# Kernel optimization log

Hardware: AMD Instinct MI355X
Metric: run time of the kernel (lower is better)

Reference implementation:

```python
import jax, jax.numpy as jnp
import numpy as np

N_NODES = 50000
N_EDGES = 640000
D_IN = 128
D_HID = 128
D_OUT = 128
N_GRAPHS = 64


def gcn_conv(x, edge_index, W, b, n_nodes):
    """PyG GCNConv: D^{-1/2} (A + I) D^{-1/2} X W + b (unit edge weights)."""
    src, dst = edge_index[0], edge_index[1]
    h = x @ W  # [N, d_out]
    # degree counts target-side edges plus the self loop
    deg = jax.ops.segment_sum(jnp.ones_like(dst, dtype=h.dtype), dst,
                              num_segments=n_nodes) + 1.0
    dinv = jax.lax.rsqrt(deg)  # deg >= 1 so always finite
    norm = dinv[src] * dinv[dst]  # [E]
    msg = h[src] * norm[:, None]  # gather + scale  [E, d_out]
    agg = jax.ops.segment_sum(msg, dst, num_segments=n_nodes)
    # self-loop contribution: norm_ii = dinv_i^2
    agg = agg + h * (dinv * dinv)[:, None]
    return agg + b


def global_mean_pool(x, batch, n_graphs):
    sums = jax.ops.segment_sum(x, batch, num_segments=n_graphs)
    cnt = jax.ops.segment_sum(jnp.ones((x.shape[0],), dtype=x.dtype), batch,
                              num_segments=n_graphs)
    return sums / jnp.maximum(cnt, 1.0)[:, None]


def setup_inputs() -> dict:
    key = jax.random.key(0)
    k = jax.random.split(key, 8)
    x = jax.random.normal(k[0], (N_NODES, D_IN), dtype=jnp.float32)
    edge_index = jax.random.randint(k[1], (2, N_EDGES), 0, N_NODES, dtype=jnp.int64)
    batch = jnp.sort(jax.random.randint(k[2], (N_NODES,), 0, N_GRAPHS, dtype=jnp.int64))
    s1 = 1.0 / np.sqrt(D_IN)
    s2 = 1.0 / np.sqrt(D_HID)
    W1 = jax.random.uniform(k[3], (D_IN, D_HID), jnp.float32, -s1, s1)
    b1 = jnp.zeros((D_HID,), jnp.float32)
    W2 = jax.random.uniform(k[4], (D_HID, D_OUT), jnp.float32, -s2, s2)
    b2 = jnp.zeros((D_OUT,), jnp.float32)
    return {"x": x, "edge_index": edge_index, "batch": batch,
            "W1": W1, "b1": b1, "W2": W2, "b2": b2}


def reference(x, edge_index, batch, W1, b1, W2, b2):
    n = x.shape[0]
    h = jax.nn.relu(gcn_conv(x, edge_index, W1, b1, n))
    h = gcn_conv(h, edge_index, W2, b2, n)
    return global_mean_pool(h, batch, N_GRAPHS)
```

## Files before the change

### kernel.cpp

```cpp
#include <hip/hip_runtime.h>


#define D 128
#define NGRAPH 64
#define AGG_BLOCKS 2048
#define BUCK_SH 9
#define BUCK_W  512
#define MAXBUCK 128

typedef _Float16 h16x2 __attribute__((ext_vector_type(2)));
typedef _Float16 f16x8 __attribute__((ext_vector_type(8)));
typedef float    f32x4 __attribute__((ext_vector_type(4)));
typedef unsigned short u16x8 __attribute__((ext_vector_type(8)));

__device__ __forceinline__ float2 h2f(unsigned u) {
    h16x2 h = __builtin_bit_cast(h16x2, u);
    return make_float2((float)h.x, (float)h.y);
}
__device__ __forceinline__ unsigned f2h(float x, float y) {
    h16x2 h;
    h.x = (_Float16)x;
    h.y = (_Float16)y;
    return __builtin_bit_cast(unsigned, h);
}

__global__ void zero_out_kernel(float* __restrict__ out, int n) {
    int i = blockIdx.x * blockDim.x + threadIdx.x;
    if (i < n) out[i] = 0.f;
}

__global__ __launch_bounds__(256) void pack_scatter_kernel(const float* __restrict__ W1,
                                                           _Float16* __restrict__ WB,
                                                           const int* __restrict__ ei,
                                                           int* __restrict__ bcnt,
                                                           unsigned* __restrict__ buck,
                                                           unsigned* __restrict__ Gz,
                                                           unsigned* __restrict__ Hz,
                                                           int N, int E, int CAP) {
    int b = (int)blockIdx.x;
    int t = (int)threadIdx.x;
    if (b < 8) {
        int idx = b * 256 + t;
        int lane = idx & 63;
        int nt   = (idx >> 6) & 7;
        int kt   = idx >> 9;
        int col  = nt * 16 + (lane & 15);
        int krow = kt * 32 + (lane >> 4) * 8;
#pragma unroll
        for (int j = 0; j < 8; ++j)
            WB[idx * 8 + j] = (_Float16)W1[(krow + j) * D + col];
        return;
    }
    if (b == 8) {
        if (t < 64)       Gz[(size_t)N * 64 + t] = 0u;
        else if (t < 128) Hz[(size_t)N * 64 + (t - 64)] = 0u;
        return;
    }
    __shared__ unsigned histL[MAXBUCK];
    __shared__ int      baseL[MAXBUCK];
    if (t < MAXBUCK) histL[t] = 0u;
    __syncthreads();

    int e0 = (b - 9) * 1024;
    int bid[4];
    unsigned lidx[4], pk[4];
#pragma unroll
    for (int j = 0; j < 4; ++j) {
        int e = e0 + t + j * 256;
        bid[j] = -1;
        if (e < E) {
            int s = ei[e];
            int d = ei[E + e];
            if (d >= 0 && d < N) {
                s = min(max(s, 0), N - 1);
                bid[j] = d >> BUCK_SH;
                pk[j]  = ((unsigned)d << 16) | (unsigned)s;
            }
        }
    }
#pragma unroll
    for (int j = 0; j < 4; ++j)
        if (bid[j] >= 0) lidx[j] = atomicAdd(&histL[bid[j]], 1u);
    __syncthreads();
    if (t < MAXBUCK && histL[t] > 0u)
        baseL[t] = atomicAdd(&bcnt[t], (int)histL[t]);
    __syncthreads();
#pragma unroll
    for (int j = 0; j < 4; ++j)
        if (bid[j] >= 0) {
            int slot = baseL[bid[j]] + (int)lidx[j];
            if (slot < CAP) buck[(size_t)bid[j] * CAP + slot] = pk[j];
        }
}

__global__ __launch_bounds__(256) void bucket_deg_kernel(const unsigned* __restrict__ buck,
                                                         const int* __restrict__ bcnt,
                                                         int* __restrict__ deg,
                                                         float* __restrict__ dinv,
                                                         int* __restrict__ padsum,
                                                         int N, int CAP) {
    __shared__ int degL[BUCK_W];
    __shared__ int red[256];
    int b = (int)blockIdx.x;
    int t = (int)threadIdx.x;
    for (int k = t; k < BUCK_W; k += 256) degL[k] = 0;
    __syncthreads();
    int cnt = min(bcnt[b], CAP);
    const unsigned* bp = buck + (size_t)b * CAP;
    for (int i = t; i < cnt; i += 256)
        atomicAdd(&degL[(bp[i] >> 16) & (BUCK_W - 1)], 1);
    __syncthreads();
    int base = b << BUCK_SH;
    int local = 0;
    for (int k = t; k < BUCK_W; k += 256) {
        int d = base + k;
        if (d < N) {
            int dg = degL[k];
            deg[d]  = dg;
            dinv[d] = rsqrtf((float)dg + 1.0f);
            local  += (dg + 7) & ~7;
        }
    }
    red[t] = local;
    __syncthreads();
    for (int off = 128; off > 0; off >>= 1) {
        if (t < off) red[t] += red[t + off];
        __syncthreads();
    }
    if (t == 0) padsum[b] = red[0];
}

__global__ __launch_bounds__(128) void bucket_scan_kernel(const int* __restrict__ padsum,
                                                          int* __restrict__ bbase,
                                                          int* __restrict__ rowstart,
                                                          int N, int nbuck) {
    __shared__ int s[128];
    int t = (int)threadIdx.x;
    int own = (t < nbuck) ? padsum[t] : 0;
    s[t] = own;
    __syncthreads();
    for (int off = 1; off < 128; off <<= 1) {
        int v = (t >= off) ? s[t - off] : 0;
        __syncthreads();
        s[t] += v;
        __syncthreads();
    }
    if (t < nbuck) bbase[t] = s[t] - own;
    if (t == 127) rowstart[N] = s[127];
}

__global__ __launch_bounds__(256) void gemm_fill_kernel(const float* __restrict__ X,
                                                        const _Float16* __restrict__ WB,
                                                        const float* __restrict__ dinv,
                                                        _Float16* __restrict__ Gh,
                                                        const unsigned* __restrict__ buck,
                                                        const int* __restrict__ bcnt,
                                                        const int* __restrict__ deg,
                                                        const int* __restrict__ bbase,
                                                        int* __restrict__ rowstart,
                                                        unsigned short* __restrict__ colidx,
                                                        int N, int CAP, int gb) {
    if ((int)blockIdx.x >= gb) {
        __shared__ int degS[BUCK_W];
        __shared__ int loff[BUCK_W];
        __shared__ int sc[256];
        int b = (int)blockIdx.x - gb;
        int t = (int)threadIdx.x;
        int base_d = b << BUCK_SH;
        for (int k = t; k < BUCK_W; k += 256) {
            int d = base_d + k;
            degS[k] = (d < N) ? deg[d] : 0;
        }
        __syncthreads();
        int p0 = (degS[2 * t] + 7) & ~7;
        int p1 = (degS[2 * t + 1] + 7) & ~7;
        int own = p0 + p1;
        sc[t] = own;
        __syncthreads();
        for (int off = 1; off < 256; off <<= 1) {
            int v = (t >= off) ? sc[t - off] : 0;
            __syncthreads();
            sc[t] += v;
            __syncthreads();
        }
        int excl = sc[t] - own;
        loff[2 * t]     = excl;
        loff[2 * t + 1] = excl + p0;
        __syncthreads();
        int bb = bbase[b];
        for (int k = t; k < BUCK_W; k += 256) {
            int d = base_d + k;
            if (d < N) {
                int rs = bb + loff[k];
                rowstart[d] = rs;
                int dg = degS[k];
                int p8 = (dg + 7) & ~7;
                for (int j = dg; j < p8; ++j)
                    colidx[rs + j] = (unsigned short)N;
            }
        }
        __syncthreads();
        for (int k = t; k < BUCK_W; k += 256) degS[k] = bb + loff[k];
        __syncthreads();
        int cnt = min(bcnt[b], CAP);
        const unsigned* bp = buck + (size_t)b * CAP;
        for (int i = t; i < cnt; i += 256) {
            unsigned u = bp[i];
            int ld = (int)((u >> 16) & (BUCK_W - 1));
            int slot = atomicAdd(&degS[ld], 1);
            colidx[slot] = (unsigned short)(u & 0xffffu);
        }
        return;
    }

    int t = (int)threadIdx.x;
    int wave = t >> 6, lane = t & 63;
    int mbase = blockIdx.x * 64 + wave * 16;
    int arow  = mbase + (lane & 15);
    if (arow >= N) arow = N - 1;
    int kgrp  = lane >> 4;

    f16x8 afrag[4];
#pragma unroll
    for (int kt = 0; kt < 4; ++kt) {
        const float* xp = X + (size_t)arow * D + kt * 32 + kgrp * 8;
        float4 a0 = *(const float4*)xp;
        float4 a1 = *(const float4*)(xp + 4);
        f16x8 af;
        af[0] = (_Float16)a0.x; af[1] = (_Float16)a0.y;
        af[2] = (_Float16)a0.z; af[3] = (_Float16)a0.w;
        af[4] = (_Float16)a1.x; af[5] = (_Float16)a1.y;
        af[6] = (_Float16)a1.z; af[7] = (_Float16)a1.w;
        afrag[kt] = af;
    }
    f32x4 acc[8];
#pragma unroll
    for (int nt = 0; nt < 8; ++nt) acc[nt] = (f32x4){0.f, 0.f, 0.f, 0.f};
#pragma unroll
    for (int kt = 0; kt < 4; ++kt) {
#pragma unroll
        for (int nt = 0; nt < 8; ++nt) {
            uint4 u = *(const uint4*)(WB + (((kt * 8 + nt) * 64 + lane) * 8));
            f16x8 bfrag = __builtin_bit_cast(f16x8, u);
            acc[nt] = __builtin_amdgcn_mfma_f32_16x16x32_f16(afrag[kt], bfrag, acc[nt], 0, 0, 0);
        }
    }
    int r0 = mbase + kgrp * 4;
#pragma unroll
    for (int r = 0; r < 4; ++r) {
        int row = r0 + r;
        if (row < N) {
            float dv = dinv[row];
#pragma unroll
            for (int nt = 0; nt < 8; ++nt)
                Gh[(size_t)row * D + nt * 16 + (lane & 15)] = (_Float16)(dv * acc[nt][r]);
        }
    }
}

__global__ __launch_bounds__(256) void agg1_kernel(const unsigned* __restrict__ Gh,
                                                   const int* __restrict__ rowstart,
                                                   const unsigned short* __restrict__ colidx,
                                                   const float* __restrict__ dinv,
                                                   const float* __restrict__ b1,
                                                   unsigned* __restrict__ Hh,
                                                   int N, int chunk) {
    int gid  = blockIdx.x * 4 + (threadIdx.x >> 6);
    int lane = threadIdx.x & 63;
    int i0 = gid * chunk, i1 = min(i0 + chunk, N);
    float bx = b1[2 * lane], by = b1[2 * lane + 1];
    for (int i = i0; i < i1; ++i) {
        float di = dinv[i];
        float2 acc = h2f(Gh[(size_t)i * 64 + lane]);
        int e0 = rowstart[i], e1 = rowstart[i + 1];
        for (int e = e0; e < e1; e += 8) {
            u16x8 cc = *(const u16x8*)(colidx + e);
            unsigned u[8];
#pragma unroll
            for (int j = 0; j < 8; ++j)
                u[j] = Gh[(size_t)cc[j] * 64 + lane];
#pragma unroll
            for (int j = 0; j < 8; ++j) {
                float2 v = h2f(u[j]);
                acc.x += v.x;
                acc.y += v.y;
            }
        }
        float hx = fmaxf(fmaf(di, acc.x, bx), 0.f) * di;
        float hy = fmaxf(fmaf(di, acc.y, by), 0.f) * di;
        Hh[(size_t)i * 64 + lane] = f2h(hx, hy);
    }
}

__global__ __launch_bounds__(256) void agg2_pool_kernel(const unsigned* __restrict__ Hh,
                                                        const int* __restrict__ rowstart,
                                                        const unsigned short* __restrict__ colidx,
                                                        const float* __restrict__ dinv,
                                                        const int* __restrict__ batch,
                                                        float* __restrict__ pool,
                                                        int N, int chunk) {
    int gid  = blockIdx.x * 4 + (threadIdx.x >> 6);
    int lane = threadIdx.x & 63;
    int i0 = gid * chunk, i1 = min(i0 + chunk, N);
    if (i0 >= N) return;

    float2 pa = make_float2(0.f, 0.f);
    int cur = min(max(batch[i0], 0), NGRAPH - 1);
    for (int i = i0; i < i1; ++i) {
        float di = dinv[i];
        float2 a = h2f(Hh[(size_t)i * 64 + lane]);
        int e0 = rowstart[i], e1 = rowstart[i + 1];
        for (int e = e0; e < e1; e += 8) {
            u16x8 cc = *(const u16x8*)(colidx + e);
            unsigned u[8];
#pragma unroll
            for (int j = 0; j < 8; ++j)
                u[j] = Hh[(size_t)cc[j] * 64 + lane];
#pragma unroll
            for (int j = 0; j < 8; ++j) {
                float2 v = h2f(u[j]);
                a.x += v.x;
                a.y += v.y;
            }
        }
        int b = min(max(batch[i], 0), NGRAPH - 1);
        if (b != cur) {
            atomicAdd(&pool[(size_t)cur * D + 2 * lane], pa.x);
            atomicAdd(&pool[(size_t)cur * D + 2 * lane + 1], pa.y);
            pa = make_float2(0.f, 0.f);
            cur = b;
        }
        pa.x = fmaf(di, a.x, pa.x);
        pa.y = fmaf(di, a.y, pa.y);
    }
    atomicAdd(&pool[(size_t)cur * D + 2 * lane], pa.x);
    atomicAdd(&pool[(size_t)cur * D + 2 * lane + 1], pa.y);
}

__device__ __forceinline__ int lbound(const int* __restrict__ a, int n, int v) {
    int lo = 0, hi = n;
    while (lo < hi) {
        int m = (lo + hi) >> 1;
        if (a[m] < v) lo = m + 1; else hi = m;
    }
    return lo;
}

__global__ void final_gemm_kernel(const float* __restrict__ pool,
                                  const int* __restrict__ batch,
                                  const float* __restrict__ W2,
                                  const float* __restrict__ b2,
                                  float* __restrict__ out, int N) {
    int g = blockIdx.x, o = threadIdx.x;
    int s = lbound(batch, N, g);
    int e = lbound(batch, N, g + 1);
    float inv_cnt = 1.0f / fmaxf((float)(e - s), 1.0f);
    float acc = 0.f;
#pragma unroll 4
    for (int k = 0; k < D; ++k)
        acc = fmaf(pool[g * D + k], W2[k * D + o], acc);
    out[g * D + o] = acc * inv_cnt + b2[o];
}


extern "C" void kernel_launch(void* const* d_in, const int* in_sizes, int n_in,
                              void* d_out, int out_size, void* d_ws, size_t ws_size,
                              hipStream_t stream) {
    const float* x     = (const float*)d_in[0];
    const int*   ei    = (const int*)  d_in[1];
    const int*   batch = (const int*)  d_in[2];
    const float* W1    = (const float*)d_in[3];
    const float* b1    = (const float*)d_in[4];
    const float* W2    = (const float*)d_in[5];
    const float* b2    = (const float*)d_in[6];
    float* out = (float*)d_out;

    const int N = in_sizes[0] / D;
    const int E = in_sizes[1] / 2;
    const int nbuck = (N + BUCK_W - 1) >> BUCK_SH;
    const int CAP   = (E / (nbuck > 0 ? nbuck : 1)) * 2 + 1024;

    char* ws = (char*)d_ws;
    size_t off = 0;
    auto carve = [&](size_t bytes) {
        size_t o = off;
        off = (off + bytes + 255) & ~(size_t)255;
        return o;
    };
    size_t o_bcnt     = carve((size_t)MAXBUCK * 4);
    size_t o_pool     = carve((size_t)NGRAPH * D * 4);
    size_t zspan      = off;
    size_t o_rowstart = carve((size_t)(N + 1) * 4);
    size_t o_deg      = carve((size_t)N * 4);
    size_t o_dinv     = carve((size_t)N * 4);
    size_t o_padsum   = carve((size_t)MAXBUCK * 4);
    size_t o_bbase    = carve((size_t)MAXBUCK * 4);
    size_t o_colidx   = carve(((size_t)E + 7 * (size_t)N + 64) * 2);
    size_t o_buck     = carve((size_t)nbuck * CAP * 4);
    size_t o_wb       = carve((size_t)D * D * 2);
    size_t o_gh       = carve((size_t)(N + 1) * D * 2);
    size_t o_hh       = carve((size_t)(N + 1) * D * 2);
    size_t need = off;

    if (ws_size < need) {
        zero_out_kernel<<<(out_size + 255) / 256, 256, 0, stream>>>(out, out_size);
        return;
    }

    int*            bcnt     = (int*)           (ws + o_bcnt);
    float*          pool     = (float*)         (ws + o_pool);
    int*            rowstart = (int*)           (ws + o_rowstart);
    int*            deg      = (int*)           (ws + o_deg);
    float*          dinv     = (float*)         (ws + o_dinv);
    int*            padsum   = (int*)           (ws + o_padsum);
    int*            bbase    = (int*)           (ws + o_bbase);
    unsigned short* colidx   = (unsigned short*)(ws + o_colidx);
    unsigned*       buck     = (unsigned*)      (ws + o_buck);
    _Float16*       WB       = (_Float16*)      (ws + o_wb);
    _Float16*       Gh       = (_Float16*)      (ws + o_gh);
    _Float16*       Hh       = (_Float16*)      (ws + o_hh);

    hipMemsetAsync(ws, 0, zspan, stream);

    int ebs = (E + 1023) / 1024;
    int gb  = (N + 63) / 64;

    pack_scatter_kernel<<<9 + ebs, 256, 0, stream>>>(W1, WB, ei, bcnt, buck,
                                                     (unsigned*)Gh, (unsigned*)Hh,
                                                     N, E, CAP);
    bucket_deg_kernel<<<nbuck, 256, 0, stream>>>(buck, bcnt, deg, dinv, padsum, N, CAP);
    bucket_scan_kernel<<<1, 128, 0, stream>>>(padsum, bbase, rowstart, N, nbuck);
    gemm_fill_kernel<<<gb + nbuck, 256, 0, stream>>>(x, WB, dinv, Gh, buck, bcnt,
                                                     deg, bbase, rowstart, colidx,
                                                     N, CAP, gb);

    int groups = AGG_BLOCKS * 4;
    int chunk  = (N + groups - 1) / groups;
    agg1_kernel<<<AGG_BLOCKS, 256, 0, stream>>>((const unsigned*)Gh, rowstart, colidx,
                                                dinv, b1, (unsigned*)Hh, N, chunk);
    agg2_pool_kernel<<<AGG_BLOCKS, 256, 0, stream>>>((const unsigned*)Hh, rowstart, colidx,
                                                     dinv, batch, pool, N, chunk);
    final_gemm_kernel<<<NGRAPH, D, 0, stream>>>(pool, batch, W2, b2, out, N);
}
```

Before: 196.4 us.

## Split feature matrices into column panels and fuse bucket scan into degree kernel

Stores the fp16 feature matrices G and H as four 32-column panels so each block's gathers touch only a 64-byte slice per neighbor, which is meant to improve cache locality. Within a wavefront, four 16-lane groups each gather a different pair of neighbors and combine their partial sums with shuffles. The separate single-block scan kernel is folded into bucket_deg using a last-block ticket, which removes one launch. Each block now handles one panel over more rows, so the per-node serial loop gets longer, and the edge-index loads are repeated across panels.

Result: slower. 269.6 us (+37.2%).

```diff
diff --git a/kernel.cpp b/kernel.cpp
--- a/kernel.cpp
+++ b/kernel.cpp
@@ -4,6 +4,7 @@
 #define D 128
 #define NGRAPH 64
 #define AGG_BLOCKS 2048
+#define NPAN 4
 #define BUCK_SH 9
 #define BUCK_W  512
 #define MAXBUCK 128
@@ -52,8 +53,14 @@
         return;
     }
     if (b == 8) {
-        if (t < 64)       Gz[(size_t)N * 64 + t] = 0u;
-        else if (t < 128) Hz[(size_t)N * 64 + (t - 64)] = 0u;
+        size_t Nrow = (size_t)N + 1;
+        if (t < 64) {
+            int p = t >> 4, k = t & 15;
+            Gz[((size_t)p * Nrow + N) * 16 + k] = 0u;
+        } else if (t < 128) {
+            int q = t - 64, p = q >> 4, k = q & 15;
+            Hz[((size_t)p * Nrow + N) * 16 + k] = 0u;
+        }
         return;
     }
     __shared__ unsigned histL[MAXBUCK];
@@ -98,9 +105,13 @@
                                                          int* __restrict__ deg,
                                                          float* __restrict__ dinv,
                                                          int* __restrict__ padsum,
-                                                         int N, int CAP) {
+                                                         int* __restrict__ bbase,
+                                                         int* __restrict__ rowstart,
+                                                         int* __restrict__ ticket,
+                                                         int N, int CAP, int nbuck) {
     __shared__ int degL[BUCK_W];
     __shared__ int red[256];
+    __shared__ int lastFlag;
     int b = (int)blockIdx.x;
     int t = (int)threadIdx.x;
     for (int k = t; k < BUCK_W; k += 256) degL[k] = 0;
@@ -128,25 +139,24 @@
         __syncthreads();
     }
     if (t == 0) padsum[b] = red[0];
-}
-
-__global__ __launch_bounds__(128) void bucket_scan_kernel(const int* __restrict__ padsum,
-                                                          int* __restrict__ bbase,
-                                                          int* __restrict__ rowstart,
-                                                          int N, int nbuck) {
-    __shared__ int s[128];
-    int t = (int)threadIdx.x;
-    int own = (t < nbuck) ? padsum[t] : 0;
-    s[t] = own;
-    __syncthreads();
-    for (int off = 1; off < 128; off <<= 1) {
-        int v = (t >= off) ? s[t - off] : 0;
-        __syncthreads();
-        s[t] += v;
-        __syncthreads();
-    }
-    if (t < nbuck) bbase[t] = s[t] - own;
-    if (t == 127) rowstart[N] = s[127];
+    __threadfence();
+    if (t == 0) lastFlag = (atomicAdd(ticket, 1) == nbuck - 1) ? 1 : 0;
+    __syncthreads();
+    if (lastFlag) {
+        __threadfence();
+        __shared__ int s[128];
+        int own = (t < nbuck) ? padsum[t] : 0;
+        if (t < 128) s[t] = own;
+        __syncthreads();
+        for (int off = 1; off < 128; off <<= 1) {
+            int v = (t < 128 && t >= off) ? s[t - off] : 0;
+            __syncthreads();
+            if (t < 128) s[t] += v;
+            __syncthreads();
+        }
+        if (t < nbuck) bbase[t] = s[t] - own;
+        if (t == 127) rowstart[N] = s[127];
+    }
 }
 
 __global__ __launch_bounds__(256) void gemm_fill_kernel(const float* __restrict__ X,
@@ -245,6 +255,7 @@
             acc[nt] = __builtin_amdgcn_mfma_f32_16x16x32_f16(afrag[kt], bfrag, acc[nt], 0, 0, 0);
         }
     }
+    size_t Nrow = (size_t)N + 1;
     int r0 = mbase + kgrp * 4;
 #pragma unroll
     for (int r = 0; r < 4; ++r) {
@@ -252,89 +263,124 @@
         if (row < N) {
             float dv = dinv[row];
 #pragma unroll
-            for (int nt = 0; nt < 8; ++nt)
-                Gh[(size_t)row * D + nt * 16 + (lane & 15)] = (_Float16)(dv * acc[nt][r]);
-        }
-    }
-}
-
-__global__ __launch_bounds__(256) void agg1_kernel(const unsigned* __restrict__ Gh,
+            for (int nt = 0; nt < 8; ++nt) {
+                size_t adr = ((size_t)(nt >> 1) * Nrow + row) * 32 + (nt & 1) * 16 + (lane & 15);
+                Gh[adr] = (_Float16)(dv * acc[nt][r]);
+            }
+        }
+    }
+}
+
+__global__ __launch_bounds__(256) void agg1_kernel(const unsigned* __restrict__ Gp,
                                                    const int* __restrict__ rowstart,
                                                    const unsigned short* __restrict__ colidx,
                                                    const float* __restrict__ dinv,
                                                    const float* __restrict__ b1,
-                                                   unsigned* __restrict__ Hh,
+                                                   unsigned* __restrict__ Hp,
                                                    int N, int chunk) {
-    int gid  = blockIdx.x * 4 + (threadIdx.x >> 6);
-    int lane = threadIdx.x & 63;
+    int bid  = (int)blockIdx.x;
+    int p    = bid & (NPAN - 1);
+    int gid  = (bid >> 2) * 4 + ((int)threadIdx.x >> 6);
+    int lane = (int)threadIdx.x & 63;
+    int eq   = lane >> 4;
+    int cl   = lane & 15;
+    size_t Nrow = (size_t)N + 1;
+    const unsigned* P = Gp + (size_t)p * Nrow * 16;
+    unsigned*       H = Hp + (size_t)p * Nrow * 16;
+    float bx = b1[p * 32 + 2 * cl], by = b1[p * 32 + 2 * cl + 1];
     int i0 = gid * chunk, i1 = min(i0 + chunk, N);
-    float bx = b1[2 * lane], by = b1[2 * lane + 1];
+    if (i0 >= N) return;
+    int e = rowstart[i0];
     for (int i = i0; i < i1; ++i) {
         float di = dinv[i];
-        float2 acc = h2f(Gh[(size_t)i * 64 + lane]);
-        int e0 = rowstart[i], e1 = rowstart[i + 1];
-        for (int e = e0; e < e1; e += 8) {
+        int e1 = rowstart[i + 1];
+        float2 acc = make_float2(0.f, 0.f);
+        if (eq == 0) {
+            float2 v = h2f(P[(size_t)i * 16 + cl]);
+            acc.x = v.x; acc.y = v.y;
+        }
+        for (; e < e1; e += 8) {
             u16x8 cc = *(const u16x8*)(colidx + e);
-            unsigned u[8];
-#pragma unroll
-            for (int j = 0; j < 8; ++j)
-                u[j] = Gh[(size_t)cc[j] * 64 + lane];
-#pragma unroll
-            for (int j = 0; j < 8; ++j) {
-                float2 v = h2f(u[j]);
-                acc.x += v.x;
-                acc.y += v.y;
-            }
-        }
-        float hx = fmaxf(fmaf(di, acc.x, bx), 0.f) * di;
-        float hy = fmaxf(fmaf(di, acc.y, by), 0.f) * di;
-        Hh[(size_t)i * 64 + lane] = f2h(hx, hy);
-    }
-}
-
-__global__ __launch_bounds__(256) void agg2_pool_kernel(const unsigned* __restrict__ Hh,
+            int cA = (int)cc[eq];
+            int cB = (int)cc[eq + 4];
+            unsigned uA = P[(size_t)cA * 16 + cl];
+            unsigned uB = P[(size_t)cB * 16 + cl];
+            float2 vA = h2f(uA), vB = h2f(uB);
+            acc.x += vA.x + vB.x;
+            acc.y += vA.y + vB.y;
+        }
+        acc.x += __shfl_xor(acc.x, 16);
+        acc.x += __shfl_xor(acc.x, 32);
+        acc.y += __shfl_xor(acc.y, 16);
+        acc.y += __shfl_xor(acc.y, 32);
+        if (eq == 0) {
+            float hx = fmaxf(fmaf(di, acc.x, bx), 0.f) * di;
+            float hy = fmaxf(fmaf(di, acc.y, by), 0.f) * di;
+            H[(size_t)i * 16 + cl] = f2h(hx, hy);
+        }
+    }
+}
+
+__global__ __launch_bounds__(256) void agg2_pool_kernel(const unsigned* __restrict__ Hp,
                                                         const int* __restrict__ rowstart,
                                                         const unsigned short* __restrict__ colidx,
                                                         const float* __restrict__ dinv,
                                                         const int* __restrict__ batch,
                                                         float* __restrict__ pool,
                                                         int N, int chunk) {
-    int gid  = blockIdx.x * 4 + (threadIdx.x >> 6);
-    int lane = threadIdx.x & 63;
+    int bid  = (int)blockIdx.x;
+    int p    = bid & (NPAN - 1);
+    int gid  = (bid >> 2) * 4 + ((int)threadIdx.x >> 6);
+    int lane = (int)threadIdx.x & 63;
+    int eq   = lane >> 4;
+    int cl   = lane & 15;
+    size_t Nrow = (size_t)N + 1;
+    const unsigned* P = Hp + (size_t)p * Nrow * 16;
     int i0 = gid * chunk, i1 = min(i0 + chunk, N);
     if (i0 >= N) return;
 
     float2 pa = make_float2(0.f, 0.f);
     int cur = min(max(batch[i0], 0), NGRAPH - 1);
+    int e = rowstart[i0];
     for (int i = i0; i < i1; ++i) {
         float di = dinv[i];
-        float2 a = h2f(Hh[(size_t)i * 64 + lane]);
-        int e0 = rowstart[i], e1 = rowstart[i + 1];
-        for (int e = e0; e < e1; e += 8) {
+        int e1 = rowstart[i + 1];
+        float2 acc = make_float2(0.f, 0.f);
+        if (eq == 0) {
+            float2 v = h2f(P[(size_t)i * 16 + cl]);
+            acc.x = v.x; acc.y = v.y;
+        }
+        for (; e < e1; e += 8) {
             u16x8 cc = *(const u16x8*)(colidx + e);
-            unsigned u[8];
-#pragma unroll
-            for (int j = 0; j < 8; ++j)
-                u[j] = Hh[(size_t)cc[j] * 64 + lane];
-#pragma unroll
-            for (int j = 0; j < 8; ++j) {
-                float2 v = h2f(u[j]);
-                a.x += v.x;
-                a.y += v.y;
-            }
-        }
+            int cA = (int)cc[eq];
+            int cB = (int)cc[eq + 4];
+            unsigned uA = P[(size_t)cA * 16 + cl];
+            unsigned uB = P[(size_t)cB * 16 + cl];
+            float2 vA = h2f(uA), vB = h2f(uB);
+            acc.x += vA.x + vB.x;
+            acc.y += vA.y + vB.y;
+        }
+        acc.x += __shfl_xor(acc.x, 16);
+        acc.x += __shfl_xor(acc.x, 32);
+        acc.y += __shfl_xor(acc.y, 16);
+        acc.y += __shfl_xor(acc.y, 32);
+
         int b = min(max(batch[i], 0), NGRAPH - 1);
         if (b != cur) {
-            atomicAdd(&pool[(size_t)cur * D + 2 * lane], pa.x);
-            atomicAdd(&pool[(size_t)cur * D + 2 * lane + 1], pa.y);
+            if (eq == 0) {
+                atomicAdd(&pool[(size_t)cur * D + p * 32 + 2 * cl],     pa.x);
+                atomicAdd(&pool[(size_t)cur * D + p * 32 + 2 * cl + 1], pa.y);
+            }
             pa = make_float2(0.f, 0.f);
             cur = b;
         }
-        pa.x = fmaf(di, a.x, pa.x);
-        pa.y = fmaf(di, a.y, pa.y);
-    }
-    atomicAdd(&pool[(size_t)cur * D + 2 * lane], pa.x);
-    atomicAdd(&pool[(size_t)cur * D + 2 * lane + 1], pa.y);
+        pa.x = fmaf(di, acc.x, pa.x);
+        pa.y = fmaf(di, acc.y, pa.y);
+    }
+    if (eq == 0) {
+        atomicAdd(&pool[(size_t)cur * D + p * 32 + 2 * cl],     pa.x);
+        atomicAdd(&pool[(size_t)cur * D + p * 32 + 2 * cl + 1], pa.y);
+    }
 }
 
 __device__ __forceinline__ int lbound(const int* __restrict__ a, int n, int v) {
@@ -389,6 +435,7 @@
     };
     size_t o_bcnt     = carve((size_t)MAXBUCK * 4);
     size_t o_pool     = carve((size_t)NGRAPH * D * 4);
+    size_t o_ticket   = carve((size_t)256);
     size_t zspan      = off;
     size_t o_rowstart = carve((size_t)(N + 1) * 4);
     size_t o_deg      = carve((size_t)N * 4);
@@ -409,6 +456,7 @@
 
     int*            bcnt     = (int*)           (ws + o_bcnt);
     float*          pool     = (float*)         (ws + o_pool);
+    int*            ticket   = (int*)           (ws + o_ticket);
     int*            rowstart = (int*)           (ws + o_rowstart);
     int*            deg      = (int*)           (ws + o_deg);
     float*          dinv     = (float*)         (ws + o_dinv);
@@ -428,14 +476,14 @@
     pack_scatter_kernel<<<9 + ebs, 256, 0, stream>>>(W1, WB, ei, bcnt, buck,
                                                      (unsigned*)Gh, (unsigned*)Hh,
                                                      N, E, CAP);
-    bucket_deg_kernel<<<nbuck, 256, 0, stream>>>(buck, bcnt, deg, dinv, padsum, N, CAP);
-    bucket_scan_kernel<<<1, 128, 0, stream>>>(padsum, bbase, rowstart, N, nbuck);
+    bucket_deg_kernel<<<nbuck, 256, 0, stream>>>(buck, bcnt, deg, dinv, padsum,
+                                                 bbase, rowstart, ticket,
+                                                 N, CAP, nbuck);
     gemm_fill_kernel<<<gb + nbuck, 256, 0, stream>>>(x, WB, dinv, Gh, buck, bcnt,
                                                      deg, bbase, rowstart, colidx,
                                                      N, CAP, gb);
 
-    int groups = AGG_BLOCKS * 4;
-    int chunk  = (N + groups - 1) / groups;
+    int chunk = (N + AGG_BLOCKS - 1) / AGG_BLOCKS;
     agg1_kernel<<<AGG_BLOCKS, 256, 0, stream>>>((const unsigned*)Gh, rowstart, colidx,
                                                 dinv, b1, (unsigned*)Hh, N, chunk);
     agg2_pool_kernel<<<AGG_BLOCKS, 256, 0, stream>>>((const unsigned*)Hh, rowstart, colidx,
```

## Fuse bucket scan into degree kernel and unroll aggregation gathers with fdot2

Applied to the files above, without the earlier changes.

Merges the single-block prefix-scan kernel into the bucket degree kernel using a last-block ticket counter, which removes one kernel launch. The aggregation loops in both GCN layers now gather 16 neighbours per iteration instead of 8, use 32-bit unsigned index arithmetic, and accumulate fp16 pairs via the fdot2 builtin instead of separate converts and adds. Together these aim to cut launch overhead, raise memory-level parallelism in the gathers and trim the ALU work per element. The cost is more registers per thread and a threadfence/atomic handshake in the degree kernel.

New measurement: 201.4 us. +2.5%, slower.

```diff
diff --git a/kernel.cpp b/kernel.cpp
--- a/kernel.cpp
+++ b/kernel.cpp
@@ -22,6 +22,18 @@
     h.x = (_Float16)x;
     h.y = (_Float16)y;
     return __builtin_bit_cast(unsigned, h);
+}
+__device__ __forceinline__ void fmix2(float& ax, float& ay, unsigned u) {
+    h16x2 h = __builtin_bit_cast(h16x2, u);
+#if __has_builtin(__builtin_amdgcn_fdot2)
+    const h16x2 onelo = {(_Float16)1.0f, (_Float16)0.0f};
+    const h16x2 onehi = {(_Float16)0.0f, (_Float16)1.0f};
+    ax = __builtin_amdgcn_fdot2(h, onelo, ax, false);
+    ay = __builtin_amdgcn_fdot2(h, onehi, ay, false);
+#else
+    ax += (float)h.x;
+    ay += (float)h.y;
+#endif
 }
 
 __global__ void zero_out_kernel(float* __restrict__ out, int n) {
@@ -98,9 +110,13 @@
                                                          int* __restrict__ deg,
                                                          float* __restrict__ dinv,
                                                          int* __restrict__ padsum,
-                                                         int N, int CAP) {
+                                                         int* __restrict__ bbase,
+                                                         int* __restrict__ rowstart,
+                                                         int* __restrict__ ticket,
+                                                         int N, int CAP, int nbuck) {
     __shared__ int degL[BUCK_W];
     __shared__ int red[256];
+    __shared__ int lastFlag;
     int b = (int)blockIdx.x;
     int t = (int)threadIdx.x;
     for (int k = t; k < BUCK_W; k += 256) degL[k] = 0;
@@ -128,25 +144,24 @@
         __syncthreads();
     }
     if (t == 0) padsum[b] = red[0];
-}
-
-__global__ __launch_bounds__(128) void bucket_scan_kernel(const int* __restrict__ padsum,
-                                                          int* __restrict__ bbase,
-                                                          int* __restrict__ rowstart,
-                                                          int N, int nbuck) {
-    __shared__ int s[128];
-    int t = (int)threadIdx.x;
-    int own = (t < nbuck) ? padsum[t] : 0;
-    s[t] = own;
-    __syncthreads();
-    for (int off = 1; off < 128; off <<= 1) {
-        int v = (t >= off) ? s[t - off] : 0;
-        __syncthreads();
-        s[t] += v;
-        __syncthreads();
-    }
-    if (t < nbuck) bbase[t] = s[t] - own;
-    if (t == 127) rowstart[N] = s[127];
+    __threadfence();
+    if (t == 0) lastFlag = (atomicAdd(ticket, 1) == nbuck - 1) ? 1 : 0;
+    __syncthreads();
+    if (lastFlag) {
+        __threadfence();
+        __shared__ int s[128];
+        int own = (t < nbuck) ? padsum[t] : 0;
+        if (t < 128) s[t] = own;
+        __syncthreads();
+        for (int off = 1; off < 128; off <<= 1) {
+            int v = (t < 128 && t >= off) ? s[t - off] : 0;
+            __syncthreads();
+            if (t < 128) s[t] += v;
+            __syncthreads();
+        }
+        if (t < nbuck) bbase[t] = s[t] - own;
+        if (t == 127) rowstart[N] = s[127];
+    }
 }
 
 __global__ __launch_bounds__(256) void gemm_fill_kernel(const float* __restrict__ X,
@@ -266,29 +281,40 @@
                                                    unsigned* __restrict__ Hh,
                                                    int N, int chunk) {
     int gid  = blockIdx.x * 4 + (threadIdx.x >> 6);
-    int lane = threadIdx.x & 63;
+    unsigned lane = threadIdx.x & 63;
     int i0 = gid * chunk, i1 = min(i0 + chunk, N);
     float bx = b1[2 * lane], by = b1[2 * lane + 1];
     for (int i = i0; i < i1; ++i) {
         float di = dinv[i];
-        float2 acc = h2f(Gh[(size_t)i * 64 + lane]);
+        float ax = 0.f, ay = 0.f;
+        fmix2(ax, ay, Gh[((unsigned)i << 6) + lane]);
         int e0 = rowstart[i], e1 = rowstart[i + 1];
-        for (int e = e0; e < e1; e += 8) {
+        int e = e0;
+        for (; e + 15 < e1; e += 16) {
+            u16x8 c0 = *(const u16x8*)(colidx + e);
+            u16x8 c1 = *(const u16x8*)(colidx + e + 8);
+            unsigned u[16];
+#pragma unroll
+            for (int j = 0; j < 8; ++j)
+                u[j] = Gh[((unsigned)c0[j] << 6) + lane];
+#pragma unroll
+            for (int j = 0; j < 8; ++j)
+                u[8 + j] = Gh[((unsigned)c1[j] << 6) + lane];
+#pragma unroll
+            for (int j = 0; j < 16; ++j) fmix2(ax, ay, u[j]);
+        }
+        for (; e < e1; e += 8) {
             u16x8 cc = *(const u16x8*)(colidx + e);
             unsigned u[8];
 #pragma unroll
             for (int j = 0; j < 8; ++j)
-                u[j] = Gh[(size_t)cc[j] * 64 + lane];
-#pragma unroll
-            for (int j = 0; j < 8; ++j) {
-                float2 v = h2f(u[j]);
-                acc.x += v.x;
-                acc.y += v.y;
-            }
-        }
-        float hx = fmaxf(fmaf(di, acc.x, bx), 0.f) * di;
-        float hy = fmaxf(fmaf(di, acc.y, by), 0.f) * di;
-        Hh[(size_t)i * 64 + lane] = f2h(hx, hy);
+                u[j] = Gh[((unsigned)cc[j] << 6) + lane];
+#pragma unroll
+            for (int j = 0; j < 8; ++j) fmix2(ax, ay, u[j]);
+        }
+        float hx = fmaxf(fmaf(di, ax, bx), 0.f) * di;
+        float hy = fmaxf(fmaf(di, ay, by), 0.f) * di;
+        Hh[((unsigned)i << 6) + lane] = f2h(hx, hy);
     }
 }
 
@@ -300,7 +326,7 @@
                                                         float* __restrict__ pool,
                                                         int N, int chunk) {
     int gid  = blockIdx.x * 4 + (threadIdx.x >> 6);
-    int lane = threadIdx.x & 63;
+    unsigned lane = threadIdx.x & 63;
     int i0 = gid * chunk, i1 = min(i0 + chunk, N);
     if (i0 >= N) return;
 
@@ -308,20 +334,31 @@
     int cur = min(max(batch[i0], 0), NGRAPH - 1);
     for (int i = i0; i < i1; ++i) {
         float di = dinv[i];
-        float2 a = h2f(Hh[(size_t)i * 64 + lane]);
+        float ax = 0.f, ay = 0.f;
+        fmix2(ax, ay, Hh[((unsigned)i << 6) + lane]);
         int e0 = rowstart[i], e1 = rowstart[i + 1];
-        for (int e = e0; e < e1; e += 8) {
+        int e = e0;
+        for (; e + 15 < e1; e += 16) {
+            u16x8 c0 = *(const u16x8*)(colidx + e);
+            u16x8 c1 = *(const u16x8*)(colidx + e + 8);
+            unsigned u[16];
+#pragma unroll
+            for (int j = 0; j < 8; ++j)
+                u[j] = Hh[((unsigned)c0[j] << 6) + lane];
+#pragma unroll
+            for (int j = 0; j < 8; ++j)
+                u[8 + j] = Hh[((unsigned)c1[j] << 6) + lane];
+#pragma unroll
+            for (int j = 0; j < 16; ++j) fmix2(ax, ay, u[j]);
+        }
+        for (; e < e1; e += 8) {
             u16x8 cc = *(const u16x8*)(colidx + e);
             unsigned u[8];
 #pragma unroll
             for (int j = 0; j < 8; ++j)
-                u[j] = Hh[(size_t)cc[j] * 64 + lane];
-#pragma unroll
-            for (int j = 0; j < 8; ++j) {
-                float2 v = h2f(u[j]);
-                a.x += v.x;
-                a.y += v.y;
-            }
+                u[j] = Hh[((unsigned)cc[j] << 6) + lane];
+#pragma unroll
+            for (int j = 0; j < 8; ++j) fmix2(ax, ay, u[j]);
         }
         int b = min(max(batch[i], 0), NGRAPH - 1);
         if (b != cur) {
@@ -330,8 +367,8 @@
             pa = make_float2(0.f, 0.f);
             cur = b;
         }
-        pa.x = fmaf(di, a.x, pa.x);
-        pa.y = fmaf(di, a.y, pa.y);
+        pa.x = fmaf(di, ax, pa.x);
+        pa.y = fmaf(di, ay, pa.y);
     }
     atomicAdd(&pool[(size_t)cur * D + 2 * lane], pa.x);
     atomicAdd(&pool[(size_t)cur * D + 2 * lane + 1], pa.y);
@@ -389,6 +426,7 @@
     };
     size_t o_bcnt     = carve((size_t)MAXBUCK * 4);
     size_t o_pool     = carve((size_t)NGRAPH * D * 4);
+    size_t o_ticket   = carve((size_t)256);
     size_t zspan      = off;
     size_t o_rowstart = carve((size_t)(N + 1) * 4);
     size_t o_deg      = carve((size_t)N * 4);
@@ -409,6 +447,7 @@
 
     int*            bcnt     = (int*)           (ws + o_bcnt);
     float*          pool     = (float*)         (ws + o_pool);
+    int*            ticket   = (int*)           (ws + o_ticket);
     int*            rowstart = (int*)           (ws + o_rowstart);
     int*            deg      = (int*)           (ws + o_deg);
     float*          dinv     = (float*)         (ws + o_dinv);
@@ -428,8 +467,9 @@
     pack_scatter_kernel<<<9 + ebs, 256, 0, stream>>>(W1, WB, ei, bcnt, buck,
                                                      (unsigned*)Gh, (unsigned*)Hh,
                                                      N, E, CAP);
-    bucket_deg_kernel<<<nbuck, 256, 0, stream>>>(buck, bcnt, deg, dinv, padsum, N, CAP);
-    bucket_scan_kernel<<<1, 128, 0, stream>>>(padsum, bbase, rowstart, N, nbuck);
+    bucket_deg_kernel<<<nbuck, 256, 0, stream>>>(buck, bcnt, deg, dinv, padsum,
+                                                 bbase, rowstart, ticket,
+                                                 N, CAP, nbuck);
     gemm_fill_kernel<<<gb + nbuck, 256, 0, stream>>>(x, WB, dinv, Gh, buck, bcnt,
                                                      deg, bbase, rowstart, colidx,
                                                      N, CAP, gb);
```

## Fold scan and final GEMM into predecessor kernels via last-block tickets

Applied to the files above, without the earlier changes.

The bucket scan is merged into bucket_deg_kernel and the final pooled GEMM into agg2_pool_kernel. In each case the last block to finish, chosen by an atomic ticket counter, does the extra work, which removes two kernel launches. The GEMM epilogue swaps the MFMA operands so each lane writes four contiguous halves with a packed uint2 store, and the aggregation kernels use 32-bit unsigned index math. The cost is that the final GEMM now runs on a single 256-thread block serially after all other blocks finish, instead of 64 parallel blocks.

Result: slower. 651.9 us (+231.9%).

```diff
diff --git a/kernel.cpp b/kernel.cpp
--- a/kernel.cpp
+++ b/kernel.cpp
@@ -98,9 +98,13 @@
                                                          int* __restrict__ deg,
                                                          float* __restrict__ dinv,
                                                          int* __restrict__ padsum,
-                                                         int N, int CAP) {
+                                                         int* __restrict__ bbase,
+                                                         int* __restrict__ rowstart,
+                                                         int* __restrict__ ticket,
+                                                         int N, int CAP, int nbuck) {
     __shared__ int degL[BUCK_W];
     __shared__ int red[256];
+    __shared__ int lastFlag;
     int b = (int)blockIdx.x;
     int t = (int)threadIdx.x;
     for (int k = t; k < BUCK_W; k += 256) degL[k] = 0;
@@ -128,25 +132,24 @@
         __syncthreads();
     }
     if (t == 0) padsum[b] = red[0];
-}
-
-__global__ __launch_bounds__(128) void bucket_scan_kernel(const int* __restrict__ padsum,
-                                                          int* __restrict__ bbase,
-                                                          int* __restrict__ rowstart,
-                                                          int N, int nbuck) {
-    __shared__ int s[128];
-    int t = (int)threadIdx.x;
-    int own = (t < nbuck) ? padsum[t] : 0;
-    s[t] = own;
-    __syncthreads();
-    for (int off = 1; off < 128; off <<= 1) {
-        int v = (t >= off) ? s[t - off] : 0;
-        __syncthreads();
-        s[t] += v;
-        __syncthreads();
-    }
-    if (t < nbuck) bbase[t] = s[t] - own;
-    if (t == 127) rowstart[N] = s[127];
+    __threadfence();
+    if (t == 0) lastFlag = (atomicAdd(ticket, 1) == nbuck - 1) ? 1 : 0;
+    __syncthreads();
+    if (lastFlag) {
+        __threadfence();
+        __shared__ int s[128];
+        int own = (t < nbuck) ? padsum[t] : 0;
+        if (t < 128) s[t] = own;
+        __syncthreads();
+        for (int off = 1; off < 128; off <<= 1) {
+            int v = (t < 128 && t >= off) ? s[t - off] : 0;
+            __syncthreads();
+            if (t < 128) s[t] += v;
+            __syncthreads();
+        }
+        if (t < nbuck) bbase[t] = s[t] - own;
+        if (t == 127) rowstart[N] = s[127];
+    }
 }
 
 __global__ __launch_bounds__(256) void gemm_fill_kernel(const float* __restrict__ X,
@@ -242,18 +245,18 @@
         for (int nt = 0; nt < 8; ++nt) {
             uint4 u = *(const uint4*)(WB + (((kt * 8 + nt) * 64 + lane) * 8));
             f16x8 bfrag = __builtin_bit_cast(f16x8, u);
-            acc[nt] = __builtin_amdgcn_mfma_f32_16x16x32_f16(afrag[kt], bfrag, acc[nt], 0, 0, 0);
-        }
-    }
-    int r0 = mbase + kgrp * 4;
-#pragma unroll
-    for (int r = 0; r < 4; ++r) {
-        int row = r0 + r;
-        if (row < N) {
-            float dv = dinv[row];
-#pragma unroll
-            for (int nt = 0; nt < 8; ++nt)
-                Gh[(size_t)row * D + nt * 16 + (lane & 15)] = (_Float16)(dv * acc[nt][r]);
+            acc[nt] = __builtin_amdgcn_mfma_f32_16x16x32_f16(bfrag, afrag[kt], acc[nt], 0, 0, 0);
+        }
+    }
+    int row = mbase + (lane & 15);
+    if (row < N) {
+        float dv = dinv[row];
+#pragma unroll
+        for (int nt = 0; nt < 8; ++nt) {
+            uint2 w;
+            w.x = f2h(dv * acc[nt][0], dv * acc[nt][1]);
+            w.y = f2h(dv * acc[nt][2], dv * acc[nt][3]);
+            *(uint2*)(Gh + (size_t)row * D + nt * 16 + kgrp * 4) = w;
         }
     }
 }
@@ -266,19 +269,19 @@
                                                    unsigned* __restrict__ Hh,
                                                    int N, int chunk) {
     int gid  = blockIdx.x * 4 + (threadIdx.x >> 6);
-    int lane = threadIdx.x & 63;
+    unsigned lane = threadIdx.x & 63;
     int i0 = gid * chunk, i1 = min(i0 + chunk, N);
     float bx = b1[2 * lane], by = b1[2 * lane + 1];
     for (int i = i0; i < i1; ++i) {
         float di = dinv[i];
-        float2 acc = h2f(Gh[(size_t)i * 64 + lane]);
+        float2 acc = h2f(Gh[((unsigned)i << 6) + lane]);
         int e0 = rowstart[i], e1 = rowstart[i + 1];
         for (int e = e0; e < e1; e += 8) {
             u16x8 cc = *(const u16x8*)(colidx + e);
             unsigned u[8];
 #pragma unroll
             for (int j = 0; j < 8; ++j)
-                u[j] = Gh[(size_t)cc[j] * 64 + lane];
+                u[j] = Gh[((unsigned)cc[j] << 6) + lane];
 #pragma unroll
             for (int j = 0; j < 8; ++j) {
                 float2 v = h2f(u[j]);
@@ -288,8 +291,17 @@
         }
         float hx = fmaxf(fmaf(di, acc.x, bx), 0.f) * di;
         float hy = fmaxf(fmaf(di, acc.y, by), 0.f) * di;
-        Hh[(size_t)i * 64 + lane] = f2h(hx, hy);
-    }
+        Hh[((unsigned)i << 6) + lane] = f2h(hx, hy);
+    }
+}
+
+__device__ __forceinline__ int lbound(const int* __restrict__ a, int n, int v) {
+    int lo = 0, hi = n;
+    while (lo < hi) {
+        int m = (lo + hi) >> 1;
+        if (a[m] < v) lo = m + 1; else hi = m;
+    }
+    return lo;
 }
 
 __global__ __launch_bounds__(256) void agg2_pool_kernel(const unsigned* __restrict__ Hh,
@@ -298,68 +310,69 @@
                                                         const float* __restrict__ dinv,
                                                         const int* __restrict__ batch,
                                                         float* __restrict__ pool,
-                                                        int N, int chunk) {
+                                                        const float* __restrict__ W2,
+                                                        const float* __restrict__ b2,
+                                                        float* __restrict__ out,
+                                                        int* __restrict__ ticket2,
+                                                        int N, int chunk, int nblk) {
     int gid  = blockIdx.x * 4 + (threadIdx.x >> 6);
-    int lane = threadIdx.x & 63;
+    unsigned lane = threadIdx.x & 63;
     int i0 = gid * chunk, i1 = min(i0 + chunk, N);
-    if (i0 >= N) return;
-
-    float2 pa = make_float2(0.f, 0.f);
-    int cur = min(max(batch[i0], 0), NGRAPH - 1);
-    for (int i = i0; i < i1; ++i) {
-        float di = dinv[i];
-        float2 a = h2f(Hh[(size_t)i * 64 + lane]);
-        int e0 = rowstart[i], e1 = rowstart[i + 1];
-        for (int e = e0; e < e1; e += 8) {
-            u16x8 cc = *(const u16x8*)(colidx + e);
-            unsigned u[8];
-#pragma unroll
-            for (int j = 0; j < 8; ++j)
-                u[j] = Hh[(size_t)cc[j] * 64 + lane];
-#pragma unroll
-            for (int j = 0; j < 8; ++j) {
-                float2 v = h2f(u[j]);
-                a.x += v.x;
-                a.y += v.y;
+
+    if (i0 < N) {
+        float2 pa = make_float2(0.f, 0.f);
+        int cur = min(max(batch[i0], 0), NGRAPH - 1);
+        for (int i = i0; i < i1; ++i) {
+            float di = dinv[i];
+            float2 a = h2f(Hh[((unsigned)i << 6) + lane]);
+            int e0 = rowstart[i], e1 = rowstart[i + 1];
+            for (int e = e0; e < e1; e += 8) {
+                u16x8 cc = *(const u16x8*)(colidx + e);
+                unsigned u[8];
+#pragma unroll
+                for (int j = 0; j < 8; ++j)
+                    u[j] = Hh[((unsigned)cc[j] << 6) + lane];
+#pragma unroll
+                for (int j = 0; j < 8; ++j) {
+                    float2 v = h2f(u[j]);
+                    a.x += v.x;
+                    a.y += v.y;
+                }
             }
-        }
-        int b = min(max(batch[i], 0), NGRAPH - 1);
-        if (b != cur) {
-            atomicAdd(&pool[(size_t)cur * D + 2 * lane], pa.x);
-            atomicAdd(&pool[(size_t)cur * D + 2 * lane + 1], pa.y);
-            pa = make_float2(0.f, 0.f);
-            cur = b;
-        }
-        pa.x = fmaf(di, a.x, pa.x);
-        pa.y = fmaf(di, a.y, pa.y);
-    }
-    atomicAdd(&pool[(size_t)cur * D + 2 * lane], pa.x);
-    atomicAdd(&pool[(size_t)cur * D + 2 * lane + 1], pa.y);
-}
-
-__device__ __forceinline__ int lbound(const int* __restrict__ a, int n, int v) {
-    int lo = 0, hi = n;
-    while (lo < hi) {
-        int m = (lo + hi) >> 1;
-        if (a[m] < v) lo = m + 1; else hi = m;
-    }
-    return lo;
-}
-
-__global__ void final_gemm_kernel(const float* __restrict__ pool,
-                                  const int* __restrict__ batch,
-                                  const float* __restrict__ W2,
-                                  const float* __restrict__ b2,
-                                  float* __restrict__ out, int N) {
-    int g = blockIdx.x, o = threadIdx.x;
-    int s = lbound(batch, N, g);
-    int e = lbound(batch, N, g + 1);
-    float inv_cnt = 1.0f / fmaxf((float)(e - s), 1.0f);
-    float acc = 0.f;
+            int b = min(max(batch[i], 0), NGRAPH - 1);
+            if (b != cur) {
+                atomicAdd(&pool[(size_t)cur * D + 2 * lane], pa.x);
+                atomicAdd(&pool[(size_t)cur * D + 2 * lane + 1], pa.y);
+                pa = make_float2(0.f, 0.f);
+                cur = b;
+            }
+            pa.x = fmaf(di, a.x, pa.x);
+            pa.y = fmaf(di, a.y, pa.y);
+        }
+        atomicAdd(&pool[(size_t)cur * D + 2 * lane], pa.x);
+        atomicAdd(&pool[(size_t)cur * D + 2 * lane + 1], pa.y);
+    }
+
+    __shared__ int lastF;
+    __threadfence();
+    if (threadIdx.x == 0)
+        lastF = (atomicAdd(ticket2, 1) == nblk - 1) ? 1 : 0;
+    __syncthreads();
+    if (lastF) {
+        __threadfence();
+        int t = (int)threadIdx.x;
+        for (int idx = t; idx < NGRAPH * D; idx += 256) {
+            int g = idx >> 7, o = idx & 127;
+            int s = lbound(batch, N, g);
+            int e = lbound(batch, N, g + 1);
+            float inv_cnt = 1.0f / fmaxf((float)(e - s), 1.0f);
+            float acc = 0.f;
 #pragma unroll 4
-    for (int k = 0; k < D; ++k)
-        acc = fmaf(pool[g * D + k], W2[k * D + o], acc);
-    out[g * D + o] = acc * inv_cnt + b2[o];
+            for (int k = 0; k < D; ++k)
+                acc = fmaf(pool[g * D + k], W2[k * D + o], acc);
+            out[idx] = acc * inv_cnt + b2[o];
+        }
+    }
 }
 
 
@@ -389,6 +402,8 @@
     };
     size_t o_bcnt     = carve((size_t)MAXBUCK * 4);
     size_t o_pool     = carve((size_t)NGRAPH * D * 4);
+    size_t o_ticket   = carve((size_t)256);
+    size_t o_ticket2  = carve((size_t)256);
     size_t zspan      = off;
     size_t o_rowstart = carve((size_t)(N + 1) * 4);
     size_t o_deg      = carve((size_t)N * 4);
@@ -409,6 +424,8 @@
 
     int*            bcnt     = (int*)           (ws + o_bcnt);
     float*          pool     = (float*)         (ws + o_pool);
+    int*            ticket   = (int*)           (ws + o_ticket);
+    int*            ticket2  = (int*)           (ws + o_ticket2);
     int*            rowstart = (int*)           (ws + o_rowstart);
     int*            deg      = (int*)           (ws + o_deg);
     float*          dinv     = (float*)         (ws + o_dinv);
@@ -428,8 +445,9 @@
     pack_scatter_kernel<<<9 + ebs, 256, 0, stream>>>(W1, WB, ei, bcnt, buck,
                                                      (unsigned*)Gh, (unsigned*)Hh,
                                                      N, E, CAP);
-    bucket_deg_kernel<<<nbuck, 256, 0, stream>>>(buck, bcnt, deg, dinv, padsum, N, CAP);
-    bucket_scan_kernel<<<1, 128, 0, stream>>>(padsum, bbase, rowstart, N, nbuck);
+    bucket_deg_kernel<<<nbuck, 256, 0, stream>>>(buck, bcnt, deg, dinv, padsum,
+                                                 bbase, rowstart, ticket,
+                                                 N, CAP, nbuck);
     gemm_fill_kernel<<<gb + nbuck, 256, 0, stream>>>(x, WB, dinv, Gh, buck, bcnt,
                                                      deg, bbase, rowstart, colidx,
                                                      N, CAP, gb);
@@ -439,6 +457,6 @@
     agg1_kernel<<<AGG_BLOCKS, 256, 0, stream>>>((const unsigned*)Gh, rowstart, colidx,
                                                 dinv, b1, (unsigned*)Hh, N, chunk);
     agg2_pool_kernel<<<AGG_BLOCKS, 256, 0, stream>>>((const unsigned*)Hh, rowstart, colidx,
-                                                     dinv, batch, pool, N, chunk);
-    final_gemm_kernel<<<NGRAPH, D, 0, stream>>>(pool, batch, W2, b2, out, N);
-}
+                                                     dinv, batch, pool, W2, b2, out,
+                                                     ticket2, N, chunk, AGG_BLOCKS);
+}
```
